# Performance work log

Measured on AMD Instinct MI355X. Metric: run time of the kernel, lower is better.

The kernel has to match this reference:

```python
import jax, jax.numpy as jnp
import numpy as np


def to_float8(x, exp_bits=4, mant_bits=3):
    # Faithful port of the torch to_float8: clamp exponent, round mantissa.
    max_exp = 2 ** (exp_bits - 1) - 1
    scale = 2.0 ** mant_bits
    sign = jnp.sign(x)
    xa = jnp.abs(x)
    e = jnp.clip(jnp.floor(jnp.log2(xa + 1e-08)), -max_exp, max_exp)
    p = jnp.exp2(e)
    mant_q = jnp.round((xa / p - 1.0) * scale) / scale
    return sign * (1.0 + mant_q) * p


def setup_inputs() -> dict:
    key = jax.random.key(0)
    k0, k1, k2, k3, k4 = jax.random.split(key, 5)
    Bz, Din, L, N, Dout = 32, 512, 512, 512, 512
    u = jax.random.normal(k0, (Bz, Din, L), jnp.float32)
    # |A| < 1 for a stable length-512 recurrence
    A_diag = jax.random.uniform(k1, (N,), jnp.float32, 0.0, 0.9)
    B = jax.random.normal(k2, (N, Din), jnp.float32) * (1.0 / np.sqrt(Din))
    C = jax.random.normal(k3, (Dout, N), jnp.float32) * (1.0 / np.sqrt(N))
    D = jax.random.normal(k4, (Dout, Din), jnp.float32) * (1.0 / np.sqrt(Din))
    return {"u": u, "A_diag": A_diag, "B": B, "C": C, "D": D}


def reference(u, A_diag, B, C, D):
    int_bits, mant_bits = 4, 3
    q = lambda t: to_float8(t, int_bits, mant_bits)
    A_q = q(A_diag)[None, :]          # [1, N]
    B_q, C_q, D_q = q(B), q(C), q(D)
    Bt = B_q.T                         # [Din, N]
    # row_checksum(B_q.t()): append column of row sums -> constant across steps
    right_cs = jnp.concatenate([Bt, Bt.sum(axis=1, keepdims=True)], axis=1)  # [Din, N+1]
    Bz, Din, L = u.shape
    N = A_diag.shape[0]
    u_t = jnp.transpose(u, (2, 0, 1))  # [L, Bz, Din]

    def step(state, ut):
        # col_checksum(ut): append row of column sums
        left_cs = jnp.concatenate([ut, ut.sum(axis=0, keepdims=True)], axis=0)  # [Bz+1, Din]
        prod_cs = left_cs @ right_cs                 # [Bz+1, N+1] checksum-padded matmul
        right_term = prod_cs[:-1, :-1]               # ut @ B_q.T  (ABFT mask is discarded in forward)
        state_q = q(state * A_q + right_term)        # [Bz, N]
        y = q(state_q @ C_q.T + ut @ D_q.T)          # [Bz, Dout]
        return state_q, y

    state0 = jnp.zeros((Bz, N), u.dtype)
    _, Y = jax.lax.scan(step, state0, u_t)           # [L, Bz, Dout]
    return jnp.transpose(Y, (1, 2, 0))               # [Bz, Dout, L]
```

## Files before the change

### kernel.cpp

```cpp
#include <hip/hip_runtime.h>
#include <hip/hip_bf16.h>


#define DINX 512
#define LSEQ 512
#define NDIM 512

__device__ __forceinline__ float q8(float x) {
    float xa = fabsf(x);
    float w  = __fadd_rn(xa, 1e-8f);
    int e = (int)((__float_as_uint(w) >> 23) & 0xFFu) - 127;
    e = e < -7 ? -7 : (e > 7 ? 7 : e);
    float p    = __int_as_float((unsigned)((e + 127) << 23));
    float invp = __int_as_float((unsigned)((127 - e) << 23));
    float t  = __fmul_rn(__fsub_rn(__fmul_rn(xa, invp), 1.0f), 8.0f);
    float m  = __fmul_rn(rintf(t), 0.125f);
    float r  = __fmul_rn(__fadd_rn(1.0f, m), p);
    return copysignf(r, x);
}

__global__ void quantk(const float* __restrict__ in, float* __restrict__ out, int n) {
    int i = blockIdx.x * blockDim.x + threadIdx.x;
    if (i < n) out[i] = q8(in[i]);
}

__global__ __launch_bounds__(256) void quantT3(const float* __restrict__ B,
                                               const float* __restrict__ C,
                                               const float* __restrict__ D,
                                               float* __restrict__ Bqt,
                                               float* __restrict__ Cqt,
                                               float* __restrict__ Dqt) {
    __shared__ float tl[32][33];
    const float* in = blockIdx.z == 0 ? B : (blockIdx.z == 1 ? C : D);
    float* out      = blockIdx.z == 0 ? Bqt : (blockIdx.z == 1 ? Cqt : Dqt);
    const int r0 = blockIdx.y * 32, c0 = blockIdx.x * 32;
    const int x = threadIdx.x & 31, y = threadIdx.x >> 5;
#pragma unroll
    for (int i = 0; i < 32; i += 8)
        tl[y + i][x] = q8(in[(r0 + y + i) * 512 + c0 + x]);
    __syncthreads();
#pragma unroll
    for (int i = 0; i < 32; i += 8)
        out[(c0 + y + i) * 512 + r0 + x] = tl[x][y + i];
}

__device__ __forceinline__ void gemm_pass(const float* __restrict__ X,
                                          const float* __restrict__ W,
                                          int m0, int n0, int KTOT,
                                          float (&acc)[2][4][2][4],
                                          float (*Xs)[128], float (*Ws)[128],
                                          int tid) {
    const int tx = tid & 15, ty = tid >> 4;
    const int srow = tid >> 4, sseg4 = (tid & 15) * 4;
    const float* xp = X + (size_t)srow * 512 + m0 + sseg4;
    const float* wp = W + (size_t)srow * 512 + n0 + sseg4;
    for (int k0 = 0; k0 < KTOT; k0 += 16) {
        float4 x0 = *(const float4*)xp;
        float4 x1 = *(const float4*)(xp + 64);
        float4 w0 = *(const float4*)wp;
        float4 w1 = *(const float4*)(wp + 64);
        xp += 16 * 512; wp += 16 * 512;
        __syncthreads();
        *(float4*)&Xs[srow][sseg4]      = x0;
        *(float4*)&Xs[srow][64 + sseg4] = x1;
        *(float4*)&Ws[srow][sseg4]      = w0;
        *(float4*)&Ws[srow][64 + sseg4] = w1;
        __syncthreads();
#pragma unroll
        for (int k = 0; k < 16; ++k) {
            float a[2][4], b[2][4];
            *(float4*)&a[0][0] = *(const float4*)&Xs[k][tx * 4];
            *(float4*)&a[1][0] = *(const float4*)&Xs[k][64 + tx * 4];
            *(float4*)&b[0][0] = *(const float4*)&Ws[k][ty * 4];
            *(float4*)&b[1][0] = *(const float4*)&Ws[k][64 + ty * 4];
#pragma unroll
            for (int p = 0; p < 2; ++p)
#pragma unroll
                for (int i = 0; i < 4; ++i)
#pragma unroll
                    for (int q = 0; q < 2; ++q)
#pragma unroll
                        for (int j = 0; j < 4; ++j)
                            acc[p][i][q][j] = fmaf(a[p][i], b[q][j], acc[p][i][q][j]);
        }
    }
}

__global__ __launch_bounds__(256) void gemm_R(const float* __restrict__ u,
                                              const float* __restrict__ Bqt,
                                              float* __restrict__ R) {
    __shared__ float Xs[16][128];
    __shared__ float Ws[16][128];
    const int b  = blockIdx.z;
    const int t0 = blockIdx.x * 128, n0 = blockIdx.y * 128;
    const int tid = threadIdx.x;
    const int tx = tid & 15, ty = tid >> 4;
    const float* ub = u + (size_t)b * (DINX * LSEQ);
    float acc[2][4][2][4] = {};
    gemm_pass(ub, Bqt, t0, n0, DINX, acc, Xs, Ws, tid);
    float* Rb = R + (size_t)b * (LSEQ * NDIM);
#pragma unroll
    for (int p = 0; p < 2; ++p)
#pragma unroll
        for (int i = 0; i < 4; ++i) {
            float* row = Rb + (size_t)(t0 + p * 64 + tx * 4 + i) * NDIM + n0;
            *(float4*)(row + ty * 4)      = make_float4(acc[p][i][0][0], acc[p][i][0][1],
                                                        acc[p][i][0][2], acc[p][i][0][3]);
            *(float4*)(row + 64 + ty * 4) = make_float4(acc[p][i][1][0], acc[p][i][1][1],
                                                        acc[p][i][1][2], acc[p][i][1][3]);
        }
}

__global__ __launch_bounds__(128) void recur(const float* __restrict__ R,
                                             const float* __restrict__ Aq,
                                             float* __restrict__ S) {
    __shared__ float tile[16][132];
    const int b  = blockIdx.x;
    const int n0 = blockIdx.y * 128;
    const int n  = threadIdx.x;
    const float a = Aq[n0 + n];
    const float* Rb = R + (size_t)b * (LSEQ * NDIM) + n0;
    float* Sb = S + (size_t)b * (NDIM * LSEQ) + (size_t)n0 * LSEQ;
    float s = 0.0f;
    const int c = (n & 3) * 4;
    const int rbase = n >> 2;
    for (int t0 = 0; t0 < LSEQ; t0 += 16) {
#pragma unroll
        for (int tt = 0; tt < 16; ++tt) {
            float r = Rb[(size_t)(t0 + tt) * NDIM + n];
            s = q8(__fadd_rn(__fmul_rn(s, a), r));
            tile[tt][n] = s;
        }
        __syncthreads();
#pragma unroll
        for (int p = 0; p < 4; ++p) {
            int row = p * 32 + rbase;
            float4 v = make_float4(tile[c + 0][row], tile[c + 1][row],
                                   tile[c + 2][row], tile[c + 3][row]);
            *(float4*)(Sb + (size_t)row * LSEQ + t0 + c) = v;
        }
        __syncthreads();
    }
}

__global__ __launch_bounds__(256) void gemm_Y(const float* __restrict__ u,
                                              const float* __restrict__ S,
                                              const float* __restrict__ Cqt,
                                              const float* __restrict__ Dqt,
                                              float* __restrict__ Y) {
    __shared__ float Xs[16][128];
    __shared__ float Ws[16][128];
    const int b  = blockIdx.z;
    const int t0 = blockIdx.x * 128, o0 = blockIdx.y * 128;
    const int tid = threadIdx.x;
    const int tx = tid & 15, ty = tid >> 4;
    const float* Sb = S + (size_t)b * (NDIM * LSEQ);
    const float* ub = u + (size_t)b * (DINX * LSEQ);
    float acc[2][4][2][4] = {};
    float c1[2][4][2][4];
    gemm_pass(Sb, Cqt, t0, o0, NDIM, acc, Xs, Ws, tid);
#pragma unroll
    for (int p = 0; p < 2; ++p)
#pragma unroll
        for (int i = 0; i < 4; ++i)
#pragma unroll
            for (int q = 0; q < 2; ++q)
#pragma unroll
                for (int j = 0; j < 4; ++j) {
                    c1[p][i][q][j] = acc[p][i][q][j];
                    acc[p][i][q][j] = 0.0f;
                }
    gemm_pass(ub, Dqt, t0, o0, DINX, acc, Xs, Ws, tid);

    float* Yb = Y + (size_t)b * (NDIM * LSEQ);
#pragma unroll
    for (int q = 0; q < 2; ++q)
#pragma unroll
        for (int j = 0; j < 4; ++j) {
            float y0[4], y1[4];
#pragma unroll
            for (int i = 0; i < 4; ++i) {
                y0[i] = q8(__fadd_rn(c1[0][i][q][j], acc[0][i][q][j]));
                y1[i] = q8(__fadd_rn(c1[1][i][q][j], acc[1][i][q][j]));
            }
            float* row = Yb + (size_t)(o0 + q * 64 + ty * 4 + j) * LSEQ + t0;
            *(float4*)(row + tx * 4)      = make_float4(y0[0], y0[1], y0[2], y0[3]);
            *(float4*)(row + 64 + tx * 4) = make_float4(y1[0], y1[1], y1[2], y1[3]);
        }
}

extern "C" void kernel_launch(void* const* d_in, const int* in_sizes, int n_in,
                              void* d_out, int out_size, void* d_ws, size_t ws_size,
                              hipStream_t stream) {
    const float* u = (const float*)d_in[0];
    const float* A = (const float*)d_in[1];
    const float* B = (const float*)d_in[2];
    const float* C = (const float*)d_in[3];
    const float* D = (const float*)d_in[4];

    float* ws  = (float*)d_ws;
    float* Aq  = ws;
    float* Bqt = Aq + 512;
    float* Cqt = Bqt + 262144;
    float* Dqt = Cqt + 262144;
    float* R   = Dqt + 262144;
    float* S   = R + 8388608;
    float* Y   = (float*)d_out;

    quantk<<<2, 256, 0, stream>>>(A, Aq, 512);
    quantT3<<<dim3(16, 16, 3), 256, 0, stream>>>(B, C, D, Bqt, Cqt, Dqt);

    gemm_R<<<dim3(4, 4, 32), 256, 0, stream>>>(u, Bqt, R);
    recur<<<dim3(32, 4), 128, 0, stream>>>(R, Aq, S);
    gemm_Y<<<dim3(4, 4, 32), 256, 0, stream>>>(u, S, Cqt, Dqt, Y);
}
```

Before: 407.9 us.

## Double the per-thread microtile and prefetch the next k-tile into registers

```diff
diff --git a/kernel.cpp b/kernel.cpp
--- a/kernel.cpp
+++ b/kernel.cpp
@@ -47,36 +47,50 @@
 __device__ __forceinline__ void gemm_pass(const float* __restrict__ X,
                                           const float* __restrict__ W,
                                           int m0, int n0, int KTOT,
-                                          float (&acc)[2][4][2][4],
+                                          float (&acc)[2][8][2][4],
                                           float (*Xs)[128], float (*Ws)[128],
                                           int tid) {
-    const int tx = tid & 15, ty = tid >> 4;
-    const int srow = tid >> 4, sseg4 = (tid & 15) * 4;
-    const float* xp = X + (size_t)srow * 512 + m0 + sseg4;
-    const float* wp = W + (size_t)srow * 512 + n0 + sseg4;
-    for (int k0 = 0; k0 < KTOT; k0 += 16) {
-        float4 x0 = *(const float4*)xp;
-        float4 x1 = *(const float4*)(xp + 64);
-        float4 w0 = *(const float4*)wp;
-        float4 w1 = *(const float4*)(wp + 64);
-        xp += 16 * 512; wp += 16 * 512;
-        __syncthreads();
-        *(float4*)&Xs[srow][sseg4]      = x0;
-        *(float4*)&Xs[srow][64 + sseg4] = x1;
-        *(float4*)&Ws[srow][sseg4]      = w0;
-        *(float4*)&Ws[srow][64 + sseg4] = w1;
-        __syncthreads();
+    const int tx = tid & 7, ty = tid >> 3;
+    const int srow = tid >> 3, scol = (tid & 7) * 4;
+    const float* xp = X + (size_t)srow * 512 + m0 + scol;
+    const float* wp = W + (size_t)srow * 512 + n0 + scol;
+    float4 px[4], pw[4];
+#pragma unroll
+    for (int j = 0; j < 4; ++j) {
+        px[j] = *(const float4*)(xp + j * 32);
+        pw[j] = *(const float4*)(wp + j * 32);
+    }
+    const int NT = KTOT / 16;
+    for (int t = 0; t < NT; ++t) {
+        __syncthreads();
+#pragma unroll
+        for (int j = 0; j < 4; ++j) {
+            *(float4*)&Xs[srow][scol + j * 32] = px[j];
+            *(float4*)&Ws[srow][scol + j * 32] = pw[j];
+        }
+        __syncthreads();
+        if (t + 1 < NT) {
+            const float* xn = xp + (size_t)(t + 1) * 16 * 512;
+            const float* wn = wp + (size_t)(t + 1) * 16 * 512;
+#pragma unroll
+            for (int j = 0; j < 4; ++j) {
+                px[j] = *(const float4*)(xn + j * 32);
+                pw[j] = *(const float4*)(wn + j * 32);
+            }
+        }
 #pragma unroll
         for (int k = 0; k < 16; ++k) {
-            float a[2][4], b[2][4];
-            *(float4*)&a[0][0] = *(const float4*)&Xs[k][tx * 4];
-            *(float4*)&a[1][0] = *(const float4*)&Xs[k][64 + tx * 4];
+            float a[2][8], b[2][4];
+            *(float4*)&a[0][0] = *(const float4*)&Xs[k][tx * 8];
+            *(float4*)&a[0][4] = *(const float4*)&Xs[k][tx * 8 + 4];
+            *(float4*)&a[1][0] = *(const float4*)&Xs[k][64 + tx * 8];
+            *(float4*)&a[1][4] = *(const float4*)&Xs[k][64 + tx * 8 + 4];
             *(float4*)&b[0][0] = *(const float4*)&Ws[k][ty * 4];
             *(float4*)&b[1][0] = *(const float4*)&Ws[k][64 + ty * 4];
 #pragma unroll
             for (int p = 0; p < 2; ++p)
 #pragma unroll
-                for (int i = 0; i < 4; ++i)
+                for (int i = 0; i < 8; ++i)
 #pragma unroll
                     for (int q = 0; q < 2; ++q)
 #pragma unroll
@@ -86,24 +100,24 @@
     }
 }
 
-__global__ __launch_bounds__(256) void gemm_R(const float* __restrict__ u,
-                                              const float* __restrict__ Bqt,
-                                              float* __restrict__ R) {
+__global__ __launch_bounds__(128, 1) void gemm_R(const float* __restrict__ u,
+                                                 const float* __restrict__ Bqt,
+                                                 float* __restrict__ R) {
     __shared__ float Xs[16][128];
     __shared__ float Ws[16][128];
     const int b  = blockIdx.z;
     const int t0 = blockIdx.x * 128, n0 = blockIdx.y * 128;
     const int tid = threadIdx.x;
-    const int tx = tid & 15, ty = tid >> 4;
+    const int tx = tid & 7, ty = tid >> 3;
     const float* ub = u + (size_t)b * (DINX * LSEQ);
-    float acc[2][4][2][4] = {};
+    float acc[2][8][2][4] = {};
     gemm_pass(ub, Bqt, t0, n0, DINX, acc, Xs, Ws, tid);
     float* Rb = R + (size_t)b * (LSEQ * NDIM);
 #pragma unroll
     for (int p = 0; p < 2; ++p)
 #pragma unroll
-        for (int i = 0; i < 4; ++i) {
-            float* row = Rb + (size_t)(t0 + p * 64 + tx * 4 + i) * NDIM + n0;
+        for (int i = 0; i < 8; ++i) {
+            float* row = Rb + (size_t)(t0 + p * 64 + tx * 8 + i) * NDIM + n0;
             *(float4*)(row + ty * 4)      = make_float4(acc[p][i][0][0], acc[p][i][0][1],
                                                         acc[p][i][0][2], acc[p][i][0][3]);
             *(float4*)(row + 64 + ty * 4) = make_float4(acc[p][i][1][0], acc[p][i][1][1],
@@ -143,26 +157,26 @@
     }
 }
 
-__global__ __launch_bounds__(256) void gemm_Y(const float* __restrict__ u,
-                                              const float* __restrict__ S,
-                                              const float* __restrict__ Cqt,
-                                              const float* __restrict__ Dqt,
-                                              float* __restrict__ Y) {
+__global__ __launch_bounds__(128, 1) void gemm_Y(const float* __restrict__ u,
+                                                 const float* __restrict__ S,
+                                                 const float* __restrict__ Cqt,
+                                                 const float* __restrict__ Dqt,
+                                                 float* __restrict__ Y) {
     __shared__ float Xs[16][128];
     __shared__ float Ws[16][128];
     const int b  = blockIdx.z;
     const int t0 = blockIdx.x * 128, o0 = blockIdx.y * 128;
     const int tid = threadIdx.x;
-    const int tx = tid & 15, ty = tid >> 4;
+    const int tx = tid & 7, ty = tid >> 3;
     const float* Sb = S + (size_t)b * (NDIM * LSEQ);
     const float* ub = u + (size_t)b * (DINX * LSEQ);
-    float acc[2][4][2][4] = {};
-    float c1[2][4][2][4];
+    float acc[2][8][2][4] = {};
+    float c1[2][8][2][4];
     gemm_pass(Sb, Cqt, t0, o0, NDIM, acc, Xs, Ws, tid);
 #pragma unroll
     for (int p = 0; p < 2; ++p)
 #pragma unroll
-        for (int i = 0; i < 4; ++i)
+        for (int i = 0; i < 8; ++i)
 #pragma unroll
             for (int q = 0; q < 2; ++q)
 #pragma unroll
@@ -177,15 +191,16 @@
     for (int q = 0; q < 2; ++q)
 #pragma unroll
         for (int j = 0; j < 4; ++j) {
-            float y0[4], y1[4];
-#pragma unroll
-            for (int i = 0; i < 4; ++i) {
-                y0[i] = q8(__fadd_rn(c1[0][i][q][j], acc[0][i][q][j]));
-                y1[i] = q8(__fadd_rn(c1[1][i][q][j], acc[1][i][q][j]));
+            float* row = Yb + (size_t)(o0 + q * 64 + ty * 4 + j) * LSEQ + t0;
+#pragma unroll
+            for (int p = 0; p < 2; ++p) {
+                float y[8];
+#pragma unroll
+                for (int i = 0; i < 8; ++i)
+                    y[i] = q8(__fadd_rn(c1[p][i][q][j], acc[p][i][q][j]));
+                *(float4*)(row + p * 64 + tx * 8)     = make_float4(y[0], y[1], y[2], y[3]);
+                *(float4*)(row + p * 64 + tx * 8 + 4) = make_float4(y[4], y[5], y[6], y[7]);
             }
-            float* row = Yb + (size_t)(o0 + q * 64 + ty * 4 + j) * LSEQ + t0;
-            *(float4*)(row + tx * 4)      = make_float4(y0[0], y0[1], y0[2], y0[3]);
-            *(float4*)(row + 64 + tx * 4) = make_float4(y1[0], y1[1], y1[2], y1[3]);
         }
 }
 
@@ -210,7 +225,7 @@
     quantk<<<2, 256, 0, stream>>>(A, Aq, 512);
     quantT3<<<dim3(16, 16, 3), 256, 0, stream>>>(B, C, D, Bqt, Cqt, Dqt);
 
-    gemm_R<<<dim3(4, 4, 32), 256, 0, stream>>>(u, Bqt, R);
+    gemm_R<<<dim3(4, 4, 32), 128, 0, stream>>>(u, Bqt, R);
     recur<<<dim3(32, 4), 128, 0, stream>>>(R, Aq, S);
-    gemm_Y<<<dim3(4, 4, 32), 256, 0, stream>>>(u, S, Cqt, Dqt, Y);
-}
+    gemm_Y<<<dim3(4, 4, 32), 128, 0, stream>>>(u, S, Cqt, Dqt, Y);
+}
```

Result: slower. 742.0 us (+81.9%).

## Store quantized weights and state in fp16 and transpose R layout for recurrence

Applied to the files above, without the earlier changes.

```diff
diff --git a/kernel.cpp b/kernel.cpp
--- a/kernel.cpp
+++ b/kernel.cpp
@@ -1,10 +1,9 @@
 #include <hip/hip_runtime.h>
 #include <hip/hip_bf16.h>
-
-
-#define DINX 512
-#define LSEQ 512
-#define NDIM 512
+#include <hip/hip_fp16.h>
+
+
+#define FULL 512
 
 __device__ __forceinline__ float q8(float x) {
     float xa = fabsf(x);
@@ -24,55 +23,59 @@
     if (i < n) out[i] = q8(in[i]);
 }
 
-__global__ __launch_bounds__(256) void quantT3(const float* __restrict__ B,
-                                               const float* __restrict__ C,
-                                               const float* __restrict__ D,
-                                               float* __restrict__ Bqt,
-                                               float* __restrict__ Cqt,
-                                               float* __restrict__ Dqt) {
+__global__ __launch_bounds__(256) void quantT3h(const float* __restrict__ B,
+                                                const float* __restrict__ C,
+                                                const float* __restrict__ D,
+                                                __half* __restrict__ Bqt,
+                                                __half* __restrict__ Cqt,
+                                                __half* __restrict__ Dqt) {
     __shared__ float tl[32][33];
     const float* in = blockIdx.z == 0 ? B : (blockIdx.z == 1 ? C : D);
-    float* out      = blockIdx.z == 0 ? Bqt : (blockIdx.z == 1 ? Cqt : Dqt);
+    __half* out     = blockIdx.z == 0 ? Bqt : (blockIdx.z == 1 ? Cqt : Dqt);
     const int r0 = blockIdx.y * 32, c0 = blockIdx.x * 32;
     const int x = threadIdx.x & 31, y = threadIdx.x >> 5;
 #pragma unroll
     for (int i = 0; i < 32; i += 8)
-        tl[y + i][x] = q8(in[(r0 + y + i) * 512 + c0 + x]);
+        tl[y + i][x] = q8(in[(r0 + y + i) * FULL + c0 + x]);
     __syncthreads();
 #pragma unroll
     for (int i = 0; i < 32; i += 8)
-        out[(c0 + y + i) * 512 + r0 + x] = tl[x][y + i];
-}
-
-__device__ __forceinline__ void gemm_pass(const float* __restrict__ X,
-                                          const float* __restrict__ W,
-                                          int m0, int n0, int KTOT,
-                                          float (&acc)[2][4][2][4],
-                                          float (*Xs)[128], float (*Ws)[128],
-                                          int tid) {
-    const int tx = tid & 15, ty = tid >> 4;
-    const int srow = tid >> 4, sseg4 = (tid & 15) * 4;
-    const float* xp = X + (size_t)srow * 512 + m0 + sseg4;
-    const float* wp = W + (size_t)srow * 512 + n0 + sseg4;
-    for (int k0 = 0; k0 < KTOT; k0 += 16) {
+        out[(c0 + y + i) * FULL + r0 + x] = __float2half(tl[x][y + i]);
+}
+
+__device__ __forceinline__ void pass_xf_wh(const float* __restrict__ X,
+                                           const __half* __restrict__ Wh,
+                                           int m0, int n0,
+                                           float (&acc)[2][4][2][4],
+                                           float (*Xs)[128], __half (*Ws)[128],
+                                           int tid) {
+    const int tx = tid & 15, ty = tid >> 4;
+    const int srow = tid >> 4, sseg4 = (tid & 15) * 4, hseg8 = (tid & 15) * 8;
+    const float*  xp = X  + (size_t)srow * FULL + m0 + sseg4;
+    const __half* wp = Wh + (size_t)srow * FULL + n0 + hseg8;
+    for (int k0 = 0; k0 < FULL; k0 += 16) {
         float4 x0 = *(const float4*)xp;
         float4 x1 = *(const float4*)(xp + 64);
-        float4 w0 = *(const float4*)wp;
-        float4 w1 = *(const float4*)(wp + 64);
-        xp += 16 * 512; wp += 16 * 512;
+        float4 wv = *(const float4*)wp;
+        xp += 16 * FULL; wp += 16 * FULL;
         __syncthreads();
         *(float4*)&Xs[srow][sseg4]      = x0;
         *(float4*)&Xs[srow][64 + sseg4] = x1;
-        *(float4*)&Ws[srow][sseg4]      = w0;
-        *(float4*)&Ws[srow][64 + sseg4] = w1;
+        *(float4*)&Ws[srow][hseg8]      = wv;
         __syncthreads();
 #pragma unroll
         for (int k = 0; k < 16; ++k) {
-            float a[2][4], b[2][4];
+            float a[2][4];
             *(float4*)&a[0][0] = *(const float4*)&Xs[k][tx * 4];
             *(float4*)&a[1][0] = *(const float4*)&Xs[k][64 + tx * 4];
-            *(float4*)&b[0][0] = *(const float4*)&Ws[k][ty * 4];
-            *(float4*)&b[1][0] = *(const float4*)&Ws[k][64 + ty * 4];
+            __half hb[2][4];
+            *(float2*)&hb[0][0] = *(const float2*)&Ws[k][ty * 4];
+            *(float2*)&hb[1][0] = *(const float2*)&Ws[k][64 + ty * 4];
+            float b[2][4];
+#pragma unroll
+            for (int q = 0; q < 2; ++q)
+#pragma unroll
+                for (int j = 0; j < 4; ++j) b[q][j] = __half2float(hb[q][j]);
 #pragma unroll
             for (int p = 0; p < 2; ++p)
 #pragma unroll
@@ -86,106 +89,130 @@
     }
 }
 
+__device__ __forceinline__ void pass_xh_wh(const __half* __restrict__ Xh,
+                                           const __half* __restrict__ Wh,
+                                           int m0, int n0,
+                                           float (&acc)[2][4][2][4],
+                                           __half (*Xs)[128], __half (*Ws)[128],
+                                           int tid) {
+    const int tx = tid & 15, ty = tid >> 4;
+    const int srow = tid >> 4, hseg8 = (tid & 15) * 8;
+    const __half* xp = Xh + (size_t)srow * FULL + m0 + hseg8;
+    const __half* wp = Wh + (size_t)srow * FULL + n0 + hseg8;
+    for (int k0 = 0; k0 < FULL; k0 += 16) {
+        float4 xv = *(const float4*)xp;
+        float4 wv = *(const float4*)wp;
+        xp += 16 * FULL; wp += 16 * FULL;
+        __syncthreads();
+        *(float4*)&Xs[srow][hseg8] = xv;
+        *(float4*)&Ws[srow][hseg8] = wv;
+        __syncthreads();
+#pragma unroll
+        for (int k = 0; k < 16; ++k) {
+            __half ha[2][4], hb[2][4];
+            *(float2*)&ha[0][0] = *(const float2*)&Xs[k][tx * 4];
+            *(float2*)&ha[1][0] = *(const float2*)&Xs[k][64 + tx * 4];
+            *(float2*)&hb[0][0] = *(const float2*)&Ws[k][ty * 4];
+            *(float2*)&hb[1][0] = *(const float2*)&Ws[k][64 + ty * 4];
+            float a[2][4], b[2][4];
+#pragma unroll
+            for (int p = 0; p < 2; ++p)
+#pragma unroll
+                for (int i = 0; i < 4; ++i) a[p][i] = __half2float(ha[p][i]);
+#pragma unroll
+            for (int q = 0; q < 2; ++q)
+#pragma unroll
+                for (int j = 0; j < 4; ++j) b[q][j] = __half2float(hb[q][j]);
+#pragma unroll
+            for (int p = 0; p < 2; ++p)
+#pragma unroll
+                for (int i = 0; i < 4; ++i)
+#pragma unroll
+                    for (int q = 0; q < 2; ++q)
+#pragma unroll
+                        for (int j = 0; j < 4; ++j)
+                            acc[p][i][q][j] = fmaf(a[p][i], b[q][j], acc[p][i][q][j]);
+        }
+    }
+}
+
 __global__ __launch_bounds__(256) void gemm_R(const float* __restrict__ u,
-                                              const float* __restrict__ Bqt,
-                                              float* __restrict__ R) {
-    __shared__ float Xs[16][128];
-    __shared__ float Ws[16][128];
+                                              const __half* __restrict__ Bqt,
+                                              float* __restrict__ Rp) {
+    __shared__ float  Xs[16][128];
+    __shared__ __half Ws[16][128];
     const int b  = blockIdx.z;
     const int t0 = blockIdx.x * 128, n0 = blockIdx.y * 128;
     const int tid = threadIdx.x;
     const int tx = tid & 15, ty = tid >> 4;
-    const float* ub = u + (size_t)b * (DINX * LSEQ);
     float acc[2][4][2][4] = {};
-    gemm_pass(ub, Bqt, t0, n0, DINX, acc, Xs, Ws, tid);
-    float* Rb = R + (size_t)b * (LSEQ * NDIM);
-#pragma unroll
-    for (int p = 0; p < 2; ++p)
-#pragma unroll
-        for (int i = 0; i < 4; ++i) {
-            float* row = Rb + (size_t)(t0 + p * 64 + tx * 4 + i) * NDIM + n0;
-            *(float4*)(row + ty * 4)      = make_float4(acc[p][i][0][0], acc[p][i][0][1],
-                                                        acc[p][i][0][2], acc[p][i][0][3]);
-            *(float4*)(row + 64 + ty * 4) = make_float4(acc[p][i][1][0], acc[p][i][1][1],
-                                                        acc[p][i][1][2], acc[p][i][1][3]);
-        }
-}
-
-__global__ __launch_bounds__(128) void recur(const float* __restrict__ R,
+    pass_xf_wh(u + (size_t)b * (FULL * FULL), Bqt, t0, n0, acc, Xs, Ws, tid);
+    float* Rb = Rp + (size_t)b * (FULL * FULL);
+#pragma unroll
+    for (int q = 0; q < 2; ++q)
+#pragma unroll
+        for (int j = 0; j < 4; ++j) {
+            const int n = n0 + q * 64 + ty * 4 + j;
+#pragma unroll
+            for (int p = 0; p < 2; ++p) {
+                float4 v = make_float4(acc[p][0][q][j], acc[p][1][q][j],
+                                       acc[p][2][q][j], acc[p][3][q][j]);
+                *(float4*)(Rb + (size_t)n * FULL + t0 + p * 64 + tx * 4) = v;
+            }
+        }
+}
+
+__global__ __launch_bounds__(128) void recur(const float* __restrict__ Rp,
                                              const float* __restrict__ Aq,
-                                             float* __restrict__ S) {
-    __shared__ float tile[16][132];
-    const int b  = blockIdx.x;
-    const int n0 = blockIdx.y * 128;
-    const int n  = threadIdx.x;
-    const float a = Aq[n0 + n];
-    const float* Rb = R + (size_t)b * (LSEQ * NDIM) + n0;
-    float* Sb = S + (size_t)b * (NDIM * LSEQ) + (size_t)n0 * LSEQ;
-    float s = 0.0f;
-    const int c = (n & 3) * 4;
-    const int rbase = n >> 2;
-    for (int t0 = 0; t0 < LSEQ; t0 += 16) {
-#pragma unroll
-        for (int tt = 0; tt < 16; ++tt) {
-            float r = Rb[(size_t)(t0 + tt) * NDIM + n];
-            s = q8(__fadd_rn(__fmul_rn(s, a), r));
-            tile[tt][n] = s;
-        }
-        __syncthreads();
-#pragma unroll
-        for (int p = 0; p < 4; ++p) {
-            int row = p * 32 + rbase;
-            float4 v = make_float4(tile[c + 0][row], tile[c + 1][row],
-                                   tile[c + 2][row], tile[c + 3][row]);
-            *(float4*)(Sb + (size_t)row * LSEQ + t0 + c) = v;
-        }
-        __syncthreads();
+                                             __half* __restrict__ Sh) {
+    const int b = blockIdx.x;
+    const int n = blockIdx.y * 128 + threadIdx.x;
+    const float a = Aq[n];
+    const float* r = Rp + (size_t)b * (FULL * FULL) + (size_t)n * FULL;
+    __half* s = Sh + (size_t)b * (FULL * FULL) + (size_t)n * FULL;
+    float st = 0.0f;
+    for (int t = 0; t < FULL; t += 4) {
+        float4 rv = *(const float4*)(r + t);
+        __half h[4];
+        st = q8(__fadd_rn(__fmul_rn(st, a), rv.x)); h[0] = __float2half(st);
+        st = q8(__fadd_rn(__fmul_rn(st, a), rv.y)); h[1] = __float2half(st);
+        st = q8(__fadd_rn(__fmul_rn(st, a), rv.z)); h[2] = __float2half(st);
+        st = q8(__fadd_rn(__fmul_rn(st, a), rv.w)); h[3] = __float2half(st);
+        *(float2*)(s + t) = *(float2*)h;
     }
 }
 
 __global__ __launch_bounds__(256) void gemm_Y(const float* __restrict__ u,
-                                              const float* __restrict__ S,
-                                              const float* __restrict__ Cqt,
-                                              const float* __restrict__ Dqt,
+                                              const __half* __restrict__ Sh,
+                                              const __half* __restrict__ Cqt,
+                                              const __half* __restrict__ Dqt,
                                               float* __restrict__ Y) {
-    __shared__ float Xs[16][128];
-    __shared__ float Ws[16][128];
+    __shared__ float  Xs[16][128];
+    __shared__ __half Ws[16][128];
     const int b  = blockIdx.z;
     const int t0 = blockIdx.x * 128, o0 = blockIdx.y * 128;
     const int tid = threadIdx.x;
     const int tx = tid & 15, ty = tid >> 4;
-    const float* Sb = S + (size_t)b * (NDIM * LSEQ);
-    const float* ub = u + (size_t)b * (DINX * LSEQ);
+    float c1[2][4][2][4] = {};
+    pass_xh_wh(Sh + (size_t)b * (FULL * FULL), Cqt, t0, o0, c1,
+               (__half(*)[128])Xs, Ws, tid);
     float acc[2][4][2][4] = {};
-    float c1[2][4][2][4];
-    gemm_pass(Sb, Cqt, t0, o0, NDIM, acc, Xs, Ws, tid);
-#pragma unroll
-    for (int p = 0; p < 2; ++p)
-#pragma unroll
-        for (int i = 0; i < 4; ++i)
-#pragma unroll
-            for (int q = 0; q < 2; ++q)
-#pragma unroll
-                for (int j = 0; j < 4; ++j) {
-                    c1[p][i][q][j] = acc[p][i][q][j];
-                    acc[p][i][q][j] = 0.0f;
-                }
-    gemm_pass(ub, Dqt, t0, o0, DINX, acc, Xs, Ws, tid);
-
-    float* Yb = Y + (size_t)b * (NDIM * LSEQ);
+    pass_xf_wh(u + (size_t)b * (FULL * FULL), Dqt, t0, o0, acc, Xs, Ws, tid);
+
+    float* Yb = Y + (size_t)b * (FULL * FULL);
 #pragma unroll
     for (int q = 0; q < 2; ++q)
 #pragma unroll
         for (int j = 0; j < 4; ++j) {
-            float y0[4], y1[4];
-#pragma unroll
-            for (int i = 0; i < 4; ++i) {
-                y0[i] = q8(__fadd_rn(c1[0][i][q][j], acc[0][i][q][j]));
-                y1[i] = q8(__fadd_rn(c1[1][i][q][j], acc[1][i][q][j]));
+            float* row = Yb + (size_t)(o0 + q * 64 + ty * 4 + j) * FULL + t0;
+#pragma unroll
+            for (int p = 0; p < 2; ++p) {
+                float y[4];
+#pragma unroll
+                for (int i = 0; i < 4; ++i)
+                    y[i] = q8(__fadd_rn(c1[p][i][q][j], acc[p][i][q][j]));
+                *(float4*)(row + p * 64 + tx * 4) = make_float4(y[0], y[1], y[2], y[3]);
             }
-            float* row = Yb + (size_t)(o0 + q * 64 + ty * 4 + j) * LSEQ + t0;
-            *(float4*)(row + tx * 4)      = make_float4(y0[0], y0[1], y0[2], y0[3]);
-            *(float4*)(row + 64 + tx * 4) = make_float4(y1[0], y1[1], y1[2], y1[3]);
         }
 }
 
@@ -198,19 +225,19 @@
     const float* C = (const float*)d_in[3];
     const float* D = (const float*)d_in[4];
 
-    float* ws  = (float*)d_ws;
-    float* Aq  = ws;
-    float* Bqt = Aq + 512;
-    float* Cqt = Bqt + 262144;
-    float* Dqt = Cqt + 262144;
-    float* R   = Dqt + 262144;
-    float* S   = R + 8388608;
-    float* Y   = (float*)d_out;
+    char* ws = (char*)d_ws;
+    float*  Aq  = (float*)ws;                      ws += 512 * 4;
+    __half* Bqt = (__half*)ws;                     ws += 262144 * 2;
+    __half* Cqt = (__half*)ws;                     ws += 262144 * 2;
+    __half* Dqt = (__half*)ws;                     ws += 262144 * 2;
+    float*  Rp  = (float*)ws;                      ws += 8388608 * 4;
+    __half* Sh  = (__half*)ws;
+    float*  Y   = (float*)d_out;
 
     quantk<<<2, 256, 0, stream>>>(A, Aq, 512);
-    quantT3<<<dim3(16, 16, 3), 256, 0, stream>>>(B, C, D, Bqt, Cqt, Dqt);
-
-    gemm_R<<<dim3(4, 4, 32), 256, 0, stream>>>(u, Bqt, R);
-    recur<<<dim3(32, 4), 128, 0, stream>>>(R, Aq, S);
-    gemm_Y<<<dim3(4, 4, 32), 256, 0, stream>>>(u, S, Cqt, Dqt, Y);
-}
+    quantT3h<<<dim3(16, 16, 3), 256, 0, stream>>>(B, C, D, Bqt, Cqt, Dqt);
+
+    gemm_R<<<dim3(4, 4, 32), 256, 0, stream>>>(u, Bqt, Rp);
+    recur<<<dim3(32, 4), 128, 0, stream>>>(Rp, Aq, Sh);
+    gemm_Y<<<dim3(4, 4, 32), 256, 0, stream>>>(u, Sh, Cqt, Dqt, Y);
+}
```

After: 515.1 us. 1.26x slower.
